# Performance work log

Measured on AMD Instinct MI355X. Metric: run time of the kernel, lower is better.

## Reference

```python
import jax, jax.numpy as jnp
import numpy as np

N_NODES = 100000
N_EDGES = 1600000
IN_DIM = 128
N_HID = 128


def setup_inputs() -> dict:
    key = jax.random.key(0)
    k1, k2, k3, k4 = jax.random.split(key, 4)
    node_feature = jax.random.normal(k1, (N_NODES, IN_DIM), dtype=jnp.float32)
    edge_index = jax.random.randint(k2, (2, N_EDGES), 0, N_NODES, dtype=jnp.int64)
    # GCN layer weights (glorot-ish scale)
    W1 = jax.random.normal(k3, (IN_DIM, N_HID), dtype=jnp.float32) / np.sqrt(IN_DIM)
    b1 = jnp.zeros((N_HID,), dtype=jnp.float32)
    W2 = jax.random.normal(k4, (N_HID, N_HID), dtype=jnp.float32) / np.sqrt(N_HID)
    b2 = jnp.zeros((N_HID,), dtype=jnp.float32)
    return {"node_feature": node_feature, "edge_index": edge_index,
            "W1": W1, "b1": b1, "W2": W2, "b2": b2}


def _gcn_layer(x, W, b, row, col, n_nodes):
    """GCNConv: x' = D^-1/2 (A + I) D^-1/2 (x W) + b, symmetric norm with self-loops."""
    xt = x @ W  # [N, out]
    ones = jnp.ones(row.shape[0], dtype=xt.dtype)
    deg = jnp.zeros((n_nodes,), dtype=xt.dtype).at[col].add(ones) + 1.0  # +1 self-loop
    dinv = jax.lax.rsqrt(deg)  # [N]
    norm = dinv[row] * dinv[col]  # [E]
    # gather messages from source (row), scatter-add into destination (col)
    agg = jnp.zeros_like(xt).at[col].add(xt[row] * norm[:, None])
    agg = agg + xt * (dinv * dinv)[:, None]  # self-loop contribution
    return agg + b


def reference(node_feature, edge_index, W1, b1, W2, b2):
    row, col = edge_index[0], edge_index[1]
    n = node_feature.shape[0]
    h = _gcn_layer(node_feature, W1, b1, row, col, n)
    # F.dropout with training=False is identity (eval-mode reference)
    h = _gcn_layer(h, W2, b2, row, col, n)
    return h
```

## Files before the change

kernel.cpp:

```cpp
#include <hip/hip_runtime.h>

typedef unsigned short ushort_t;
typedef __attribute__((ext_vector_type(8))) short short8;
typedef __attribute__((ext_vector_type(8))) unsigned short us8v;
typedef __attribute__((ext_vector_type(4))) float f32x4;

__device__ __forceinline__ float b2f(unsigned short u) {
    union { unsigned int i; float f; } v; v.i = ((unsigned int)u) << 16; return v.f;
}
__device__ __forceinline__ unsigned short f2b(float f) {
    union { float f; unsigned int i; } v; v.f = f;
    unsigned int r = (v.i + 0x7FFF + ((v.i >> 16) & 1)) >> 16;
    return (unsigned short)r;
}

__device__ __forceinline__ void load_edge(const int* __restrict__ ei, int e, int E,
                                          int is64, int& s, int& d) {
    if (is64) {
        const long long* el = (const long long*)ei;
        s = (int)el[e]; d = (int)el[E + e];
    } else {
        s = ei[e]; d = ei[E + e];
    }
}

__device__ __forceinline__ int detect64(const int* __restrict__ ei, int t) {
    int z = 0;
    for (int i = t; i < 512; i += 256) z |= ei[2 * i + 1];
    return (__syncthreads_or(z) == 0);
}

__global__ __launch_bounds__(256) void k_histT(const int* __restrict__ ei, int E,
                                               unsigned N, int* __restrict__ bhist,
                                               int BSH, int NB, int nch,
                                               const float* __restrict__ W1,
                                               const float* __restrict__ W2,
                                               ushort_t* __restrict__ WT) {
    __shared__ int lh[256];
    int t = threadIdx.x;
    int b = blockIdx.x;
    if (b >= nch) {
        const float* src = (b == nch) ? W1 : W2;
        ushort_t* dst = WT + (b - nch) * 16384;
        for (int i = t; i < 16384; i += 256) {
            int n = i >> 7, k = i & 127;
            dst[i] = f2b(src[k * 128 + n]);
        }
        return;
    }
    for (int q = t; q < NB; q += 256) lh[q] = 0;
    int is64 = detect64(ei, t);
    int e0 = b * 4096;
    #pragma unroll
    for (int i = 0; i < 16; ++i) {
        int e = e0 + i * 256 + t;
        if (e < E) {
            int d = is64 ? (int)((const long long*)ei)[E + e] : ei[E + e];
            if ((unsigned)d < N) atomicAdd(&lh[d >> BSH], 1);
        }
    }
    __syncthreads();
    for (int q = t; q < NB; q += 256) { int v = lh[q]; if (v) atomicAdd(&bhist[q], v); }
}

__global__ void k_scanb(const int* __restrict__ bhist, int NB,
                        int* __restrict__ bkbase, int* __restrict__ bkcur) {
    __shared__ int sd[256];
    int t = threadIdx.x;
    int v0 = (t < NB) ? bhist[t] : 0;
    sd[t] = v0;
    for (int o = 1; o < 256; o <<= 1) {
        __syncthreads();
        int v = (t >= o) ? sd[t - o] : 0;
        __syncthreads();
        sd[t] += v;
    }
    __syncthreads();
    if (t < NB) { int ex = sd[t] - v0; bkbase[t] = ex; bkcur[t] = ex; }
}

__global__ __launch_bounds__(256) void k_bg(const int* __restrict__ ei, int E,
                                            unsigned N, int* __restrict__ bkcur,
                                            int* __restrict__ bs, int* __restrict__ bd,
                                            int BSH, int NB, int nch,
                                            const float* __restrict__ x,
                                            const ushort_t* __restrict__ WT,
                                            ushort_t* __restrict__ xt, int M) {
    __shared__ __align__(16) int smem[13056];
    int t = threadIdx.x;
    int b = blockIdx.x;

    if (b < nch) {
        int* lss = smem;
        int* ldd = smem + 4096;
        int* lhist = smem + 8192;
        int* lcur = smem + 8448;
        int e0 = b * 4096;
        for (int q = t; q < NB; q += 256) lhist[q] = 0;
        int is64 = detect64(ei, t);
        #pragma unroll
        for (int i = 0; i < 16; ++i) {
            int idx = i * 256 + t, e = e0 + idx;
            int s = -1, d = -1;
            if (e < E) {
                load_edge(ei, e, E, is64, s, d);
                if (!((unsigned)s < N && (unsigned)d < N)) d = -1;
            }
            lss[idx] = s; ldd[idx] = d;
            if (d >= 0) atomicAdd(&lhist[d >> BSH], 1);
        }
        __syncthreads();
        for (int q = t; q < NB; q += 256) {
            int v = lhist[q];
            lcur[q] = v ? atomicAdd(&bkcur[q], v) : 0;
        }
        __syncthreads();
        #pragma unroll
        for (int i = 0; i < 16; ++i) {
            int idx = i * 256 + t;
            int d = ldd[idx];
            if (d >= 0) {
                int p = atomicAdd(&lcur[d >> BSH], 1);
                bs[p] = lss[idx]; bd[p] = d;
            }
        }
    } else {
        ushort_t* sA = (ushort_t*)smem;
        ushort_t* sW = (ushort_t*)smem + 8704;
        int row0 = (b - nch) * 64;
        #pragma unroll
        for (int it = 0; it < 8; ++it) {
            int flat = (it * 256 + t) * 8;
            int n = flat >> 7, k = flat & 127;
            uint4 v = *(const uint4*)(WT + flat);
            *(uint4*)(&sW[n * 136 + k]) = v;
        }
        #pragma unroll
        for (int it = 0; it < 4; ++it) {
            int flat = (it * 256 + t) * 8;
            int r = flat >> 7, cc = flat & 127;
            int row = row0 + r; if (row > M - 1) row = M - 1;
            const float* p = x + (size_t)row * 128 + cc;
            float4 f0 = *(const float4*)p;
            float4 f1 = *(const float4*)(p + 4);
            ushort_t tmp[8] __attribute__((aligned(16)));
            tmp[0] = f2b(f0.x); tmp[1] = f2b(f0.y); tmp[2] = f2b(f0.z); tmp[3] = f2b(f0.w);
            tmp[4] = f2b(f1.x); tmp[5] = f2b(f1.y); tmp[6] = f2b(f1.z); tmp[7] = f2b(f1.w);
            *(uint4*)(&sA[r * 136 + cc]) = *(const uint4*)tmp;
        }
        __syncthreads();
        int w = t >> 6, lane = t & 63;
        int m = lane & 15, quad = lane >> 4;
        f32x4 acc[8] = {};
        #pragma unroll
        for (int k0 = 0; k0 < 128; k0 += 32) {
            short8 af = *(const short8*)(&sA[(w * 16 + m) * 136 + k0 + quad * 8]);
            #pragma unroll
            for (int tt = 0; tt < 8; ++tt) {
                short8 bf = *(const short8*)(&sW[(tt * 16 + m) * 136 + k0 + quad * 8]);
                acc[tt] = __builtin_amdgcn_mfma_f32_16x16x32_bf16(af, bf, acc[tt], 0, 0, 0);
            }
        }
        #pragma unroll
        for (int r = 0; r < 4; ++r) {
            int row = row0 + w * 16 + quad * 4 + r;
            if (row < M) {
                #pragma unroll
                for (int tt = 0; tt < 8; ++tt)
                    xt[(size_t)row * 128 + tt * 16 + m] = f2b(acc[tt][r]);
            }
        }
    }
}

__global__ __launch_bounds__(256) void k_caf(const int* __restrict__ bs,
                                             const int* __restrict__ bd,
                                             const int* __restrict__ bkbase,
                                             const int* __restrict__ bkcur,
                                             int N, int BSH,
                                             int* __restrict__ pos,
                                             int* __restrict__ cnt,
                                             float* __restrict__ dinv,
                                             int* __restrict__ srcs) {
    __shared__ int lc[512];
    __shared__ int sc[512];
    int b = blockIdx.x, t = threadIdx.x;
    int nbase = b << BSH;
    int nn = min(1 << BSH, N - nbase);
    int segbase = bkbase[b] + b * (7 << BSH);

    lc[t] = 0; lc[t + 256] = 0;
    __syncthreads();
    int s0 = bkbase[b], s1 = bkcur[b];
    for (int i = s0 + t; i < s1; i += 256) atomicAdd(&lc[bd[i] - nbase], 1);
    __syncthreads();

    int c0 = (t < nn) ? lc[t] : 0;
    int c1 = (t + 256 < nn) ? lc[t + 256] : 0;
    int p0 = (c0 + 7) & ~7;
    int p1 = (c1 + 7) & ~7;
    sc[t] = p0; sc[t + 256] = p1;
    __syncthreads();
    for (int o = 1; o < 512; o <<= 1) {
        int v0 = (t >= o) ? sc[t - o] : 0;
        int v1 = (t + 256 >= o) ? sc[t + 256 - o] : 0;
        __syncthreads();
        sc[t] += v0; sc[t + 256] += v1;
        __syncthreads();
    }
    if (t < nn) {
        int st = segbase + sc[t] - p0;
        pos[nbase + t] = st;
        cnt[nbase + t] = c0;
        dinv[nbase + t] = rsqrtf((float)c0 + 1.0f);
        for (int q = c0; q < p0; ++q) srcs[st + q] = nbase + t;
        lc[t] = st;
    }
    if (t + 256 < nn) {
        int st = segbase + sc[t + 256] - p1;
        pos[nbase + t + 256] = st;
        cnt[nbase + t + 256] = c1;
        dinv[nbase + t + 256] = rsqrtf((float)c1 + 1.0f);
        for (int q = c1; q < p1; ++q) srcs[st + q] = nbase + t + 256;
        lc[t + 256] = st;
    }
    __syncthreads();
    for (int i = s0 + t; i < s1; i += 256) {
        int d = bd[i];
        int p = atomicAdd(&lc[d - nbase], 1);
        srcs[p] = bs[i];
    }
}

__global__ __launch_bounds__(256) void k_gemm2(const ushort_t* __restrict__ A,
                                               const ushort_t* __restrict__ WT,
                                               ushort_t* __restrict__ C,
                                               const float* __restrict__ dinv, int M) {
    __shared__ __align__(16) ushort_t sA[64 * 136];
    __shared__ __align__(16) ushort_t sW[128 * 136];
    int t = threadIdx.x;
    int row0 = blockIdx.x * 64;
    #pragma unroll
    for (int it = 0; it < 8; ++it) {
        int flat = (it * 256 + t) * 8;
        int n = flat >> 7, k = flat & 127;
        uint4 v = *(const uint4*)(WT + flat);
        *(uint4*)(&sW[n * 136 + k]) = v;
    }
    #pragma unroll
    for (int it = 0; it < 4; ++it) {
        int flat = (it * 256 + t) * 8;
        int r = flat >> 7, cc = flat & 127;
        int row = row0 + r; if (row > M - 1) row = M - 1;
        us8v v = *(const us8v*)(A + ((size_t)row << 7) + cc);
        *(us8v*)(&sA[r * 136 + cc]) = v;
    }
    __syncthreads();
    int w = t >> 6, lane = t & 63;
    int m = lane & 15, quad = lane >> 4;
    f32x4 acc[8] = {};
    #pragma unroll
    for (int k0 = 0; k0 < 128; k0 += 32) {
        short8 af = *(const short8*)(&sA[(w * 16 + m) * 136 + k0 + quad * 8]);
        #pragma unroll
        for (int tt = 0; tt < 8; ++tt) {
            short8 bf = *(const short8*)(&sW[(tt * 16 + m) * 136 + k0 + quad * 8]);
            acc[tt] = __builtin_amdgcn_mfma_f32_16x16x32_bf16(af, bf, acc[tt], 0, 0, 0);
        }
    }
    #pragma unroll
    for (int r = 0; r < 4; ++r) {
        int row = row0 + w * 16 + quad * 4 + r;
        if (row < M) {
            float dd = dinv[row];
            #pragma unroll
            for (int tt = 0; tt < 8; ++tt)
                C[(size_t)row * 128 + tt * 16 + m] = f2b(dd * acc[tt][r]);
        }
    }
}

template <bool OBF, bool WEI>
__global__ __launch_bounds__(256) void k_agg(const ushort_t* __restrict__ xt,
                                             const float* __restrict__ bias,
                                             void* __restrict__ outp,
                                             const int* __restrict__ pos,
                                             const int* __restrict__ cnts,
                                             const float* __restrict__ dinv,
                                             const int* __restrict__ srcs, int N) {
    int lane = threadIdx.x & 63;
    int slot = lane >> 4, j = lane & 15;
    int d = (blockIdx.x << 2) + (threadIdx.x >> 6);
    if (d >= N) return;
    int c = cnts[d];
    int cn = (c + 7) & ~7;
    float kpad = (float)(cn - c);
    int start = pos[d];
    float dd = dinv[d];
    float selfc = WEI ? (1.f - kpad) * dd * dd : (1.f - kpad) * dd;
    us8v vs = *(const us8v*)(xt + ((size_t)d << 7) + (j << 3));
    float4 bb0 = *(const float4*)(bias + (j << 3));
    float4 bb1 = *(const float4*)(bias + (j << 3) + 4);

    float a0 = 0.f, a1 = 0.f, a2 = 0.f, a3 = 0.f;
    float a4 = 0.f, a5 = 0.f, a6 = 0.f, a7 = 0.f;

    for (int base = 0; base < cn; base += 64) {
        int n = cn - base; if (n > 64) n = 64;
        int sv = 0; float wv = 1.f;
        if (lane < n) {
            sv = srcs[start + base + lane];
            if (WEI) wv = dinv[sv];
        }
        int s0 = __shfl(sv, slot);
        int s1 = __shfl(sv, 4 + slot);
        float w0 = WEI ? __shfl(wv, slot) : 1.f;
        float w1 = WEI ? __shfl(wv, 4 + slot) : 1.f;
        us8v v0 = *(const us8v*)(xt + ((size_t)s0 << 7) + (j << 3));
        us8v v1 = *(const us8v*)(xt + ((size_t)s1 << 7) + (j << 3));
        for (int cc = 8; cc < n; cc += 8) {
            int t0 = __shfl(sv, cc + slot);
            int t1 = __shfl(sv, cc + 4 + slot);
            float u0 = WEI ? __shfl(wv, cc + slot) : 1.f;
            float u1 = WEI ? __shfl(wv, cc + 4 + slot) : 1.f;
            us8v n0 = *(const us8v*)(xt + ((size_t)t0 << 7) + (j << 3));
            us8v n1 = *(const us8v*)(xt + ((size_t)t1 << 7) + (j << 3));
            if (WEI) {
                a0 += w0 * b2f(v0[0]); a1 += w0 * b2f(v0[1]);
                a2 += w0 * b2f(v0[2]); a3 += w0 * b2f(v0[3]);
                a4 += w0 * b2f(v0[4]); a5 += w0 * b2f(v0[5]);
                a6 += w0 * b2f(v0[6]); a7 += w0 * b2f(v0[7]);
                a0 += w1 * b2f(v1[0]); a1 += w1 * b2f(v1[1]);
                a2 += w1 * b2f(v1[2]); a3 += w1 * b2f(v1[3]);
                a4 += w1 * b2f(v1[4]); a5 += w1 * b2f(v1[5]);
                a6 += w1 * b2f(v1[6]); a7 += w1 * b2f(v1[7]);
            } else {
                a0 += b2f(v0[0]); a1 += b2f(v0[1]); a2 += b2f(v0[2]); a3 += b2f(v0[3]);
                a4 += b2f(v0[4]); a5 += b2f(v0[5]); a6 += b2f(v0[6]); a7 += b2f(v0[7]);
                a0 += b2f(v1[0]); a1 += b2f(v1[1]); a2 += b2f(v1[2]); a3 += b2f(v1[3]);
                a4 += b2f(v1[4]); a5 += b2f(v1[5]); a6 += b2f(v1[6]); a7 += b2f(v1[7]);
            }
            v0 = n0; v1 = n1; w0 = u0; w1 = u1;
        }
        if (WEI) {
            a0 += w0 * b2f(v0[0]); a1 += w0 * b2f(v0[1]);
            a2 += w0 * b2f(v0[2]); a3 += w0 * b2f(v0[3]);
            a4 += w0 * b2f(v0[4]); a5 += w0 * b2f(v0[5]);
            a6 += w0 * b2f(v0[6]); a7 += w0 * b2f(v0[7]);
            a0 += w1 * b2f(v1[0]); a1 += w1 * b2f(v1[1]);
            a2 += w1 * b2f(v1[2]); a3 += w1 * b2f(v1[3]);
            a4 += w1 * b2f(v1[4]); a5 += w1 * b2f(v1[5]);
            a6 += w1 * b2f(v1[6]); a7 += w1 * b2f(v1[7]);
        } else {
            a0 += b2f(v0[0]); a1 += b2f(v0[1]); a2 += b2f(v0[2]); a3 += b2f(v0[3]);
            a4 += b2f(v0[4]); a5 += b2f(v0[5]); a6 += b2f(v0[6]); a7 += b2f(v0[7]);
            a0 += b2f(v1[0]); a1 += b2f(v1[1]); a2 += b2f(v1[2]); a3 += b2f(v1[3]);
            a4 += b2f(v1[4]); a5 += b2f(v1[5]); a6 += b2f(v1[6]); a7 += b2f(v1[7]);
        }
    }
    a0 += __shfl_xor(a0, 32); a1 += __shfl_xor(a1, 32);
    a2 += __shfl_xor(a2, 32); a3 += __shfl_xor(a3, 32);
    a4 += __shfl_xor(a4, 32); a5 += __shfl_xor(a5, 32);
    a6 += __shfl_xor(a6, 32); a7 += __shfl_xor(a7, 32);
    a0 += __shfl_xor(a0, 16); a1 += __shfl_xor(a1, 16);
    a2 += __shfl_xor(a2, 16); a3 += __shfl_xor(a3, 16);
    a4 += __shfl_xor(a4, 16); a5 += __shfl_xor(a5, 16);
    a6 += __shfl_xor(a6, 16); a7 += __shfl_xor(a7, 16);

    if (slot == 0) {
        float o0 = dd * a0 + selfc * b2f(vs[0]) + bb0.x;
        float o1 = dd * a1 + selfc * b2f(vs[1]) + bb0.y;
        float o2 = dd * a2 + selfc * b2f(vs[2]) + bb0.z;
        float o3 = dd * a3 + selfc * b2f(vs[3]) + bb0.w;
        float o4 = dd * a4 + selfc * b2f(vs[4]) + bb1.x;
        float o5 = dd * a5 + selfc * b2f(vs[5]) + bb1.y;
        float o6 = dd * a6 + selfc * b2f(vs[6]) + bb1.z;
        float o7 = dd * a7 + selfc * b2f(vs[7]) + bb1.w;
        if (OBF) {
            ushort_t tmp[8] __attribute__((aligned(16)));
            tmp[0] = f2b(o0); tmp[1] = f2b(o1); tmp[2] = f2b(o2); tmp[3] = f2b(o3);
            tmp[4] = f2b(o4); tmp[5] = f2b(o5); tmp[6] = f2b(o6); tmp[7] = f2b(o7);
            *(us8v*)((ushort_t*)outp + ((size_t)d << 7) + (j << 3)) = *(const us8v*)tmp;
        } else {
            float4 q0 = { o0, o1, o2, o3 };
            float4 q1 = { o4, o5, o6, o7 };
            float4* po = (float4*)((float*)outp + ((size_t)d << 7) + (j << 3));
            po[0] = q0; po[1] = q1;
        }
    }
}


extern "C" void kernel_launch(void* const* d_in, const int* in_sizes, int n_in,
                              void* d_out, int out_size, void* d_ws, size_t ws_size,
                              hipStream_t stream) {
    const float* x  = (const float*)d_in[0];
    const int*   ei = (const int*)d_in[1];
    const float* W1 = (const float*)d_in[2];
    const float* b1 = (const float*)d_in[3];
    const float* W2 = (const float*)d_in[4];
    const float* b2 = (const float*)d_in[5];
    float* out = (float*)d_out;

    const int N = in_sizes[0] / 128;
    const int E = in_sizes[1] / 2;

    int BSH = 9;
    int NB = (N + (1 << BSH) - 1) >> BSH;
    while (NB > 256) { BSH++; NB = (N + (1 << BSH) - 1) >> BSH; }

    char* ws = (char*)d_ws;
    size_t o = 0;
    auto take = [&](size_t bytes) { size_t r = o; o = (o + bytes + 255) & ~(size_t)255; return r; };
    size_t o_bhist  = take(256 * 4);
    size_t zero_end = o;
    size_t o_bkbase = take(256 * 4);
    size_t o_bkcur  = take(256 * 4);
    size_t o_cnt    = take((size_t)N * 4);
    size_t o_pos    = take((size_t)N * 4);
    size_t o_dinv   = take((size_t)N * 4);
    size_t o_srcs   = take(((size_t)E + (size_t)NB * (7 << BSH) + 64) * 4);
    size_t o_WT     = take(2 * 128 * 128 * 2);
    size_t big_sz   = (size_t)E * 8 > (size_t)N * 256 ? (size_t)E * 8 : (size_t)N * 256;
    size_t o_big    = take(big_sz);
    (void)ws_size;

    int*      bhist  = (int*)(ws + o_bhist);
    int*      bkbase = (int*)(ws + o_bkbase);
    int*      bkcur  = (int*)(ws + o_bkcur);
    int*      cnt    = (int*)(ws + o_cnt);
    int*      pos    = (int*)(ws + o_pos);
    float*    dinv   = (float*)(ws + o_dinv);
    int*      srcs   = (int*)(ws + o_srcs);
    ushort_t* WT     = (ushort_t*)(ws + o_WT);
    int*      bs     = (int*)(ws + o_big);
    int*      bd     = (int*)(ws + o_big) + E;
    ushort_t* xt2    = (ushort_t*)(ws + o_big);
    ushort_t* xt1    = (ushort_t*)d_out;
    ushort_t* hbf    = (ushort_t*)d_out + (size_t)N * 128;

    hipMemsetAsync(d_ws, 0, zero_end, stream);

    int nch = (E + 4095) / 4096;
    int gG  = (N + 63) / 64;
    int gA  = (N + 3) / 4;
    unsigned Nu = (unsigned)N;

    k_histT<<<nch + 2, 256, 0, stream>>>(ei, E, Nu, bhist, BSH, NB, nch, W1, W2, WT);
    k_scanb<<<1, 256, 0, stream>>>(bhist, NB, bkbase, bkcur);
    k_bg<<<nch + gG, 256, 0, stream>>>(ei, E, Nu, bkcur, bs, bd, BSH, NB, nch,
                                       x, WT, xt1, N);
    k_caf<<<NB, 256, 0, stream>>>(bs, bd, bkbase, bkcur, N, BSH, pos, cnt, dinv, srcs);

    k_agg<true, true><<<gA, 256, 0, stream>>>(xt1, b1, hbf, pos, cnt, dinv, srcs, N);
    k_gemm2<<<gG, 256, 0, stream>>>(hbf, WT + 16384, xt2, dinv, N);
    k_agg<false, false><<<gA, 256, 0, stream>>>(xt2, b2, out, pos, cnt, dinv, srcs, N);
}
```

Before: 317.8 us.

## Store intermediate features in column-slab layout and aggregate per 16-feature slice

The bf16 intermediate feature matrices are now written by both GEMMs as eight slabs of 16 features per node instead of row-major 128-wide rows. The aggregation kernel assigns each block to one slab, so its gathered working set is a 1/8-sized array that can stay in cache, and each wave gathers 32-byte segments per neighbor. The aim is better L2/MALL hit rates for the random neighbor gathers. The cost is that each edge's source index and weight are read eight times, one per slice, and each gather moves smaller chunks.

```diff
diff --git a/kernel.cpp b/kernel.cpp
--- a/kernel.cpp
+++ b/kernel.cpp
@@ -4,6 +4,8 @@
 typedef __attribute__((ext_vector_type(8))) short short8;
 typedef __attribute__((ext_vector_type(8))) unsigned short us8v;
 typedef __attribute__((ext_vector_type(4))) float f32x4;
+
+struct __align__(4) us2 { unsigned short x, y; };
 
 __device__ __forceinline__ float b2f(unsigned short u) {
     union { unsigned int i; float f; } v; v.i = ((unsigned int)u) << 16; return v.f;
@@ -128,6 +130,7 @@
         ushort_t* sA = (ushort_t*)smem;
         ushort_t* sW = (ushort_t*)smem + 8704;
         int row0 = (b - nch) * 64;
+        size_t sstride = (size_t)M * 16;
         #pragma unroll
         for (int it = 0; it < 8; ++it) {
             int flat = (it * 256 + t) * 8;
@@ -167,7 +170,7 @@
             if (row < M) {
                 #pragma unroll
                 for (int tt = 0; tt < 8; ++tt)
-                    xt[(size_t)row * 128 + tt * 16 + m] = f2b(acc[tt][r]);
+                    xt[(size_t)tt * sstride + (size_t)row * 16 + m] = f2b(acc[tt][r]);
             }
         }
     }
@@ -240,6 +243,7 @@
     __shared__ __align__(16) ushort_t sW[128 * 136];
     int t = threadIdx.x;
     int row0 = blockIdx.x * 64;
+    size_t sstride = (size_t)M * 16;
     #pragma unroll
     for (int it = 0; it < 8; ++it) {
         int flat = (it * 256 + t) * 8;
@@ -252,7 +256,8 @@
         int flat = (it * 256 + t) * 8;
         int r = flat >> 7, cc = flat & 127;
         int row = row0 + r; if (row > M - 1) row = M - 1;
-        us8v v = *(const us8v*)(A + ((size_t)row << 7) + cc);
+        int slab = cc >> 4, off = cc & 15;
+        us8v v = *(const us8v*)(A + (size_t)slab * sstride + (size_t)row * 16 + off);
         *(us8v*)(&sA[r * 136 + cc]) = v;
     }
     __syncthreads();
@@ -275,7 +280,7 @@
             float dd = dinv[row];
             #pragma unroll
             for (int tt = 0; tt < 8; ++tt)
-                C[(size_t)row * 128 + tt * 16 + m] = f2b(dd * acc[tt][r]);
+                C[(size_t)tt * sstride + (size_t)row * 16 + m] = f2b(dd * acc[tt][r]);
         }
     }
 }
@@ -289,103 +294,61 @@
                                              const float* __restrict__ dinv,
                                              const int* __restrict__ srcs, int N) {
     int lane = threadIdx.x & 63;
-    int slot = lane >> 4, j = lane & 15;
-    int d = (blockIdx.x << 2) + (threadIdx.x >> 6);
-    if (d >= N) return;
-    int c = cnts[d];
-    int cn = (c + 7) & ~7;
-    float kpad = (float)(cn - c);
-    int start = pos[d];
-    float dd = dinv[d];
-    float selfc = WEI ? (1.f - kpad) * dd * dd : (1.f - kpad) * dd;
-    us8v vs = *(const us8v*)(xt + ((size_t)d << 7) + (j << 3));
-    float4 bb0 = *(const float4*)(bias + (j << 3));
-    float4 bb1 = *(const float4*)(bias + (j << 3) + 4);
-
-    float a0 = 0.f, a1 = 0.f, a2 = 0.f, a3 = 0.f;
-    float a4 = 0.f, a5 = 0.f, a6 = 0.f, a7 = 0.f;
-
-    for (int base = 0; base < cn; base += 64) {
-        int n = cn - base; if (n > 64) n = 64;
-        int sv = 0; float wv = 1.f;
-        if (lane < n) {
-            sv = srcs[start + base + lane];
-            if (WEI) wv = dinv[sv];
-        }
-        int s0 = __shfl(sv, slot);
-        int s1 = __shfl(sv, 4 + slot);
-        float w0 = WEI ? __shfl(wv, slot) : 1.f;
-        float w1 = WEI ? __shfl(wv, 4 + slot) : 1.f;
-        us8v v0 = *(const us8v*)(xt + ((size_t)s0 << 7) + (j << 3));
-        us8v v1 = *(const us8v*)(xt + ((size_t)s1 << 7) + (j << 3));
-        for (int cc = 8; cc < n; cc += 8) {
-            int t0 = __shfl(sv, cc + slot);
-            int t1 = __shfl(sv, cc + 4 + slot);
-            float u0 = WEI ? __shfl(wv, cc + slot) : 1.f;
-            float u1 = WEI ? __shfl(wv, cc + 4 + slot) : 1.f;
-            us8v n0 = *(const us8v*)(xt + ((size_t)t0 << 7) + (j << 3));
-            us8v n1 = *(const us8v*)(xt + ((size_t)t1 << 7) + (j << 3));
-            if (WEI) {
-                a0 += w0 * b2f(v0[0]); a1 += w0 * b2f(v0[1]);
-                a2 += w0 * b2f(v0[2]); a3 += w0 * b2f(v0[3]);
-                a4 += w0 * b2f(v0[4]); a5 += w0 * b2f(v0[5]);
-                a6 += w0 * b2f(v0[6]); a7 += w0 * b2f(v0[7]);
-                a0 += w1 * b2f(v1[0]); a1 += w1 * b2f(v1[1]);
-                a2 += w1 * b2f(v1[2]); a3 += w1 * b2f(v1[3]);
-                a4 += w1 * b2f(v1[4]); a5 += w1 * b2f(v1[5]);
-                a6 += w1 * b2f(v1[6]); a7 += w1 * b2f(v1[7]);
+    int wid = threadIdx.x >> 6;
+    int slice = blockIdx.x & 7;
+    int dbase = (blockIdx.x >> 3) * 16;
+    int g = lane >> 3;
+    int fp = lane & 7;
+    size_t sstride = (size_t)N * 16;
+    const ushort_t* slab = xt + (size_t)slice * sstride;
+    float2 bb = *(const float2*)(bias + slice * 16 + fp * 2);
+
+    for (int k = 0; k < 4; ++k) {
+        int d = dbase + wid + k * 4;
+        if (d >= N) break;
+        int c = cnts[d];
+        int cn = (c + 7) & ~7;
+        float kpad = (float)(cn - c);
+        int start = pos[d];
+        float dd = dinv[d];
+        float selfc = WEI ? (1.f - kpad) * dd * dd : (1.f - kpad) * dd;
+        us2 vsv = *(const us2*)(slab + (size_t)d * 16 + fp * 2);
+
+        float a0 = 0.f, a1 = 0.f;
+        for (int base = 0; base < cn; base += 64) {
+            int n = cn - base; if (n > 64) n = 64;
+            int sv = 0; float wv = 1.f;
+            if (lane < n) {
+                sv = srcs[start + base + lane];
+                if (WEI) wv = dinv[sv];
+            }
+            #pragma unroll 4
+            for (int cc = 0; cc < n; cc += 8) {
+                int s = __shfl(sv, cc + g);
+                us2 v = *(const us2*)(slab + (size_t)s * 16 + fp * 2);
+                if (WEI) {
+                    float w = __shfl(wv, cc + g);
+                    a0 += w * b2f(v.x); a1 += w * b2f(v.y);
+                } else {
+                    a0 += b2f(v.x); a1 += b2f(v.y);
+                }
+            }
+        }
+        a0 += __shfl_xor(a0, 8);  a1 += __shfl_xor(a1, 8);
+        a0 += __shfl_xor(a0, 16); a1 += __shfl_xor(a1, 16);
+        a0 += __shfl_xor(a0, 32); a1 += __shfl_xor(a1, 32);
+
+        if (g == 0) {
+            float o0 = dd * a0 + selfc * b2f(vsv.x) + bb.x;
+            float o1 = dd * a1 + selfc * b2f(vsv.y) + bb.y;
+            if (OBF) {
+                us2 t2; t2.x = f2b(o0); t2.y = f2b(o1);
+                *(us2*)((ushort_t*)outp + (size_t)slice * sstride
+                        + (size_t)d * 16 + fp * 2) = t2;
             } else {
-                a0 += b2f(v0[0]); a1 += b2f(v0[1]); a2 += b2f(v0[2]); a3 += b2f(v0[3]);
-                a4 += b2f(v0[4]); a5 += b2f(v0[5]); a6 += b2f(v0[6]); a7 += b2f(v0[7]);
-                a0 += b2f(v1[0]); a1 += b2f(v1[1]); a2 += b2f(v1[2]); a3 += b2f(v1[3]);
-                a4 += b2f(v1[4]); a5 += b2f(v1[5]); a6 += b2f(v1[6]); a7 += b2f(v1[7]);
-            }
-            v0 = n0; v1 = n1; w0 = u0; w1 = u1;
-        }
-        if (WEI) {
-            a0 += w0 * b2f(v0[0]); a1 += w0 * b2f(v0[1]);
-            a2 += w0 * b2f(v0[2]); a3 += w0 * b2f(v0[3]);
-            a4 += w0 * b2f(v0[4]); a5 += w0 * b2f(v0[5]);
-            a6 += w0 * b2f(v0[6]); a7 += w0 * b2f(v0[7]);
-            a0 += w1 * b2f(v1[0]); a1 += w1 * b2f(v1[1]);
-            a2 += w1 * b2f(v1[2]); a3 += w1 * b2f(v1[3]);
-            a4 += w1 * b2f(v1[4]); a5 += w1 * b2f(v1[5]);
-            a6 += w1 * b2f(v1[6]); a7 += w1 * b2f(v1[7]);
-        } else {
-            a0 += b2f(v0[0]); a1 += b2f(v0[1]); a2 += b2f(v0[2]); a3 += b2f(v0[3]);
-            a4 += b2f(v0[4]); a5 += b2f(v0[5]); a6 += b2f(v0[6]); a7 += b2f(v0[7]);
-            a0 += b2f(v1[0]); a1 += b2f(v1[1]); a2 += b2f(v1[2]); a3 += b2f(v1[3]);
-            a4 += b2f(v1[4]); a5 += b2f(v1[5]); a6 += b2f(v1[6]); a7 += b2f(v1[7]);
-        }
-    }
-    a0 += __shfl_xor(a0, 32); a1 += __shfl_xor(a1, 32);
-    a2 += __shfl_xor(a2, 32); a3 += __shfl_xor(a3, 32);
-    a4 += __shfl_xor(a4, 32); a5 += __shfl_xor(a5, 32);
-    a6 += __shfl_xor(a6, 32); a7 += __shfl_xor(a7, 32);
-    a0 += __shfl_xor(a0, 16); a1 += __shfl_xor(a1, 16);
-    a2 += __shfl_xor(a2, 16); a3 += __shfl_xor(a3, 16);
-    a4 += __shfl_xor(a4, 16); a5 += __shfl_xor(a5, 16);
-    a6 += __shfl_xor(a6, 16); a7 += __shfl_xor(a7, 16);
-
-    if (slot == 0) {
-        float o0 = dd * a0 + selfc * b2f(vs[0]) + bb0.x;
-        float o1 = dd * a1 + selfc * b2f(vs[1]) + bb0.y;
-        float o2 = dd * a2 + selfc * b2f(vs[2]) + bb0.z;
-        float o3 = dd * a3 + selfc * b2f(vs[3]) + bb0.w;
-        float o4 = dd * a4 + selfc * b2f(vs[4]) + bb1.x;
-        float o5 = dd * a5 + selfc * b2f(vs[5]) + bb1.y;
-        float o6 = dd * a6 + selfc * b2f(vs[6]) + bb1.z;
-        float o7 = dd * a7 + selfc * b2f(vs[7]) + bb1.w;
-        if (OBF) {
-            ushort_t tmp[8] __attribute__((aligned(16)));
-            tmp[0] = f2b(o0); tmp[1] = f2b(o1); tmp[2] = f2b(o2); tmp[3] = f2b(o3);
-            tmp[4] = f2b(o4); tmp[5] = f2b(o5); tmp[6] = f2b(o6); tmp[7] = f2b(o7);
-            *(us8v*)((ushort_t*)outp + ((size_t)d << 7) + (j << 3)) = *(const us8v*)tmp;
-        } else {
-            float4 q0 = { o0, o1, o2, o3 };
-            float4 q1 = { o4, o5, o6, o7 };
-            float4* po = (float4*)((float*)outp + ((size_t)d << 7) + (j << 3));
-            po[0] = q0; po[1] = q1;
+                float2 q; q.x = o0; q.y = o1;
+                *(float2*)((float*)outp + (size_t)d * 128 + slice * 16 + fp * 2) = q;
+            }
         }
     }
 }
@@ -443,7 +406,7 @@
 
     int nch = (E + 4095) / 4096;
     int gG  = (N + 63) / 64;
-    int gA  = (N + 3) / 4;
+    int gA  = 8 * ((N + 15) / 16);
     unsigned Nu = (unsigned)N;
 
     k_histT<<<nch + 2, 256, 0, stream>>>(ei, E, Nu, bhist, BSH, NB, nch, W1, W2, WT);
```

Result: slower. 582.0 us (+83.1%).

## Fuse bucket scan into histogram kernel and reduce CSR padding to four

Applied to the files above, without the earlier changes.

The single-block bucket scan kernel is folded into the histogram kernel using a last-block-done atomic counter, which removes one kernel launch. Per-node edge lists are now padded to multiples of 4 instead of 8, and the aggregation loop gains a 4-edge tail path. This cuts the padding gathers of self-row values (average degree is 16, so 8-padding wasted about 3.5 rows per node). The cost is an extra global atomic and fence per block, plus a bit more control flow in the aggregation loop.

```diff
diff --git a/kernel.cpp b/kernel.cpp
--- a/kernel.cpp
+++ b/kernel.cpp
@@ -35,8 +35,12 @@
                                                int BSH, int NB, int nch,
                                                const float* __restrict__ W1,
                                                const float* __restrict__ W2,
-                                               ushort_t* __restrict__ WT) {
+                                               ushort_t* __restrict__ WT,
+                                               int* __restrict__ done,
+                                               int* __restrict__ bkbase,
+                                               int* __restrict__ bkcur) {
     __shared__ int lh[256];
+    __shared__ int lastFlag;
     int t = threadIdx.x;
     int b = blockIdx.x;
     if (b >= nch) {
@@ -46,37 +50,39 @@
             int n = i >> 7, k = i & 127;
             dst[i] = f2b(src[k * 128 + n]);
         }
-        return;
-    }
-    for (int q = t; q < NB; q += 256) lh[q] = 0;
-    int is64 = detect64(ei, t);
-    int e0 = b * 4096;
-    #pragma unroll
-    for (int i = 0; i < 16; ++i) {
-        int e = e0 + i * 256 + t;
-        if (e < E) {
-            int d = is64 ? (int)((const long long*)ei)[E + e] : ei[E + e];
-            if ((unsigned)d < N) atomicAdd(&lh[d >> BSH], 1);
-        }
-    }
-    __syncthreads();
-    for (int q = t; q < NB; q += 256) { int v = lh[q]; if (v) atomicAdd(&bhist[q], v); }
-}
-
-__global__ void k_scanb(const int* __restrict__ bhist, int NB,
-                        int* __restrict__ bkbase, int* __restrict__ bkcur) {
-    __shared__ int sd[256];
-    int t = threadIdx.x;
-    int v0 = (t < NB) ? bhist[t] : 0;
-    sd[t] = v0;
-    for (int o = 1; o < 256; o <<= 1) {
-        __syncthreads();
-        int v = (t >= o) ? sd[t - o] : 0;
-        __syncthreads();
-        sd[t] += v;
-    }
-    __syncthreads();
-    if (t < NB) { int ex = sd[t] - v0; bkbase[t] = ex; bkcur[t] = ex; }
+    } else {
+        for (int q = t; q < NB; q += 256) lh[q] = 0;
+        int is64 = detect64(ei, t);
+        int e0 = b * 4096;
+        #pragma unroll
+        for (int i = 0; i < 16; ++i) {
+            int e = e0 + i * 256 + t;
+            if (e < E) {
+                int d = is64 ? (int)((const long long*)ei)[E + e] : ei[E + e];
+                if ((unsigned)d < N) atomicAdd(&lh[d >> BSH], 1);
+            }
+        }
+        __syncthreads();
+        for (int q = t; q < NB; q += 256) {
+            int v = lh[q]; if (v) atomicAdd(&bhist[q], v);
+        }
+    }
+    __threadfence();
+    if (t == 0) lastFlag = (atomicAdd(done, 1) == (int)gridDim.x - 1);
+    __syncthreads();
+    if (lastFlag) {
+        __threadfence();
+        int v0 = (t < NB) ? atomicAdd(&bhist[t], 0) : 0;
+        lh[t] = v0;
+        for (int o = 1; o < 256; o <<= 1) {
+            __syncthreads();
+            int v = (t >= o) ? lh[t - o] : 0;
+            __syncthreads();
+            lh[t] += v;
+        }
+        __syncthreads();
+        if (t < NB) { int ex = lh[t] - v0; bkbase[t] = ex; bkcur[t] = ex; }
+    }
 }
 
 __global__ __launch_bounds__(256) void k_bg(const int* __restrict__ ei, int E,
@@ -187,7 +193,7 @@
     int b = blockIdx.x, t = threadIdx.x;
     int nbase = b << BSH;
     int nn = min(1 << BSH, N - nbase);
-    int segbase = bkbase[b] + b * (7 << BSH);
+    int segbase = bkbase[b] + b * (3 << BSH);
 
     lc[t] = 0; lc[t + 256] = 0;
     __syncthreads();
@@ -197,8 +203,8 @@
 
     int c0 = (t < nn) ? lc[t] : 0;
     int c1 = (t + 256 < nn) ? lc[t + 256] : 0;
-    int p0 = (c0 + 7) & ~7;
-    int p1 = (c1 + 7) & ~7;
+    int p0 = (c0 + 3) & ~3;
+    int p1 = (c1 + 3) & ~3;
     sc[t] = p0; sc[t + 256] = p1;
     __syncthreads();
     for (int o = 1; o < 512; o <<= 1) {
@@ -293,7 +299,7 @@
     int d = (blockIdx.x << 2) + (threadIdx.x >> 6);
     if (d >= N) return;
     int c = cnts[d];
-    int cn = (c + 7) & ~7;
+    int cn = (c + 3) & ~3;
     float kpad = (float)(cn - c);
     int start = pos[d];
     float dd = dinv[d];
@@ -312,20 +318,21 @@
             sv = srcs[start + base + lane];
             if (WEI) wv = dinv[sv];
         }
-        int s0 = __shfl(sv, slot);
-        int s1 = __shfl(sv, 4 + slot);
-        float w0 = WEI ? __shfl(wv, slot) : 1.f;
-        float w1 = WEI ? __shfl(wv, 4 + slot) : 1.f;
-        us8v v0 = *(const us8v*)(xt + ((size_t)s0 << 7) + (j << 3));
-        us8v v1 = *(const us8v*)(xt + ((size_t)s1 << 7) + (j << 3));
-        for (int cc = 8; cc < n; cc += 8) {
-            int t0 = __shfl(sv, cc + slot);
-            int t1 = __shfl(sv, cc + 4 + slot);
-            float u0 = WEI ? __shfl(wv, cc + slot) : 1.f;
-            float u1 = WEI ? __shfl(wv, cc + 4 + slot) : 1.f;
-            us8v n0 = *(const us8v*)(xt + ((size_t)t0 << 7) + (j << 3));
-            us8v n1 = *(const us8v*)(xt + ((size_t)t1 << 7) + (j << 3));
-            if (WEI) {
+        int n8 = n & ~7;
+        if (n8) {
+            int s0 = __shfl(sv, slot);
+            int s1 = __shfl(sv, 4 + slot);
+            float w0 = WEI ? __shfl(wv, slot) : 1.f;
+            float w1 = WEI ? __shfl(wv, 4 + slot) : 1.f;
+            us8v v0 = *(const us8v*)(xt + ((size_t)s0 << 7) + (j << 3));
+            us8v v1 = *(const us8v*)(xt + ((size_t)s1 << 7) + (j << 3));
+            for (int cc = 8; cc < n8; cc += 8) {
+                int t0 = __shfl(sv, cc + slot);
+                int t1 = __shfl(sv, cc + 4 + slot);
+                float u0 = WEI ? __shfl(wv, cc + slot) : 1.f;
+                float u1 = WEI ? __shfl(wv, cc + 4 + slot) : 1.f;
+                us8v m0 = *(const us8v*)(xt + ((size_t)t0 << 7) + (j << 3));
+                us8v m1 = *(const us8v*)(xt + ((size_t)t1 << 7) + (j << 3));
                 a0 += w0 * b2f(v0[0]); a1 += w0 * b2f(v0[1]);
                 a2 += w0 * b2f(v0[2]); a3 += w0 * b2f(v0[3]);
                 a4 += w0 * b2f(v0[4]); a5 += w0 * b2f(v0[5]);
@@ -334,15 +341,8 @@
                 a2 += w1 * b2f(v1[2]); a3 += w1 * b2f(v1[3]);
                 a4 += w1 * b2f(v1[4]); a5 += w1 * b2f(v1[5]);
                 a6 += w1 * b2f(v1[6]); a7 += w1 * b2f(v1[7]);
-            } else {
-                a0 += b2f(v0[0]); a1 += b2f(v0[1]); a2 += b2f(v0[2]); a3 += b2f(v0[3]);
-                a4 += b2f(v0[4]); a5 += b2f(v0[5]); a6 += b2f(v0[6]); a7 += b2f(v0[7]);
-                a0 += b2f(v1[0]); a1 += b2f(v1[1]); a2 += b2f(v1[2]); a3 += b2f(v1[3]);
-                a4 += b2f(v1[4]); a5 += b2f(v1[5]); a6 += b2f(v1[6]); a7 += b2f(v1[7]);
-            }
-            v0 = n0; v1 = n1; w0 = u0; w1 = u1;
-        }
-        if (WEI) {
+                v0 = m0; v1 = m1; w0 = u0; w1 = u1;
+            }
             a0 += w0 * b2f(v0[0]); a1 += w0 * b2f(v0[1]);
             a2 += w0 * b2f(v0[2]); a3 += w0 * b2f(v0[3]);
             a4 += w0 * b2f(v0[4]); a5 += w0 * b2f(v0[5]);
@@ -351,11 +351,15 @@
             a2 += w1 * b2f(v1[2]); a3 += w1 * b2f(v1[3]);
             a4 += w1 * b2f(v1[4]); a5 += w1 * b2f(v1[5]);
             a6 += w1 * b2f(v1[6]); a7 += w1 * b2f(v1[7]);
-        } else {
-            a0 += b2f(v0[0]); a1 += b2f(v0[1]); a2 += b2f(v0[2]); a3 += b2f(v0[3]);
-            a4 += b2f(v0[4]); a5 += b2f(v0[5]); a6 += b2f(v0[6]); a7 += b2f(v0[7]);
-            a0 += b2f(v1[0]); a1 += b2f(v1[1]); a2 += b2f(v1[2]); a3 += b2f(v1[3]);
-            a4 += b2f(v1[4]); a5 += b2f(v1[5]); a6 += b2f(v1[6]); a7 += b2f(v1[7]);
+        }
+        if (n & 4) {
+            int s = __shfl(sv, n8 + slot);
+            float w = WEI ? __shfl(wv, n8 + slot) : 1.f;
+            us8v v = *(const us8v*)(xt + ((size_t)s << 7) + (j << 3));
+            a0 += w * b2f(v[0]); a1 += w * b2f(v[1]);
+            a2 += w * b2f(v[2]); a3 += w * b2f(v[3]);
+            a4 += w * b2f(v[4]); a5 += w * b2f(v[5]);
+            a6 += w * b2f(v[6]); a7 += w * b2f(v[7]);
         }
     }
     a0 += __shfl_xor(a0, 32); a1 += __shfl_xor(a1, 32);
@@ -413,19 +417,21 @@
     size_t o = 0;
     auto take = [&](size_t bytes) { size_t r = o; o = (o + bytes + 255) & ~(size_t)255; return r; };
     size_t o_bhist  = take(256 * 4);
+    size_t o_done   = take(4);
     size_t zero_end = o;
     size_t o_bkbase = take(256 * 4);
     size_t o_bkcur  = take(256 * 4);
     size_t o_cnt    = take((size_t)N * 4);
     size_t o_pos    = take((size_t)N * 4);
     size_t o_dinv   = take((size_t)N * 4);
-    size_t o_srcs   = take(((size_t)E + (size_t)NB * (7 << BSH) + 64) * 4);
+    size_t o_srcs   = take(((size_t)E + (size_t)NB * (3 << BSH) + 64) * 4);
     size_t o_WT     = take(2 * 128 * 128 * 2);
     size_t big_sz   = (size_t)E * 8 > (size_t)N * 256 ? (size_t)E * 8 : (size_t)N * 256;
     size_t o_big    = take(big_sz);
     (void)ws_size;
 
     int*      bhist  = (int*)(ws + o_bhist);
+    int*      done   = (int*)(ws + o_done);
     int*      bkbase = (int*)(ws + o_bkbase);
     int*      bkcur  = (int*)(ws + o_bkcur);
     int*      cnt    = (int*)(ws + o_cnt);
@@ -446,8 +452,8 @@
     int gA  = (N + 3) / 4;
     unsigned Nu = (unsigned)N;
 
-    k_histT<<<nch + 2, 256, 0, stream>>>(ei, E, Nu, bhist, BSH, NB, nch, W1, W2, WT);
-    k_scanb<<<1, 256, 0, stream>>>(bhist, NB, bkbase, bkcur);
+    k_histT<<<nch + 2, 256, 0, stream>>>(ei, E, Nu, bhist, BSH, NB, nch,
+                                         W1, W2, WT, done, bkbase, bkcur);
     k_bg<<<nch + gG, 256, 0, stream>>>(ei, E, Nu, bkcur, bs, bd, BSH, NB, nch,
                                        x, WT, xt1, N);
     k_caf<<<NB, 256, 0, stream>>>(bs, bd, bkbase, bkcur, N, BSH, pos, cnt, dinv, srcs);
```

Measured after the change: 335.1 us. 1.05x slower.

## Fold bucket scan into consumers and split GEMM1 across bucketing and CSR kernels

Applied to the files above, without the earlier changes.

Removes the single-block scan kernel launch: each bucketing block and each CSR-build block recomputes the 256-entry prefix scan of the bucket histogram in shared memory, and bkcur is now zeroed and holds relative offsets. The first-layer GEMM blocks are split in half, with one half co-scheduled alongside edge bucketing and the other alongside the CSR build, to fill idle CUs in the small NB-block kernel. The aggregation loop is also simplified to always apply weights. The cost is redundant scans in every block, which add extra syncs, and more shared memory in k_caf.

```diff
diff --git a/kernel.cpp b/kernel.cpp
--- a/kernel.cpp
+++ b/kernel.cpp
@@ -28,6 +28,56 @@
     int z = 0;
     for (int i = t; i < 512; i += 256) z |= ei[2 * i + 1];
     return (__syncthreads_or(z) == 0);
+}
+
+__device__ __forceinline__ void gemm1_block(const float* __restrict__ x,
+                                            const ushort_t* __restrict__ WT,
+                                            ushort_t* __restrict__ xt, int M,
+                                            int row0, int* smem, int t) {
+    ushort_t* sA = (ushort_t*)smem;
+    ushort_t* sW = (ushort_t*)smem + 8704;
+    #pragma unroll
+    for (int it = 0; it < 8; ++it) {
+        int flat = (it * 256 + t) * 8;
+        int n = flat >> 7, k = flat & 127;
+        uint4 v = *(const uint4*)(WT + flat);
+        *(uint4*)(&sW[n * 136 + k]) = v;
+    }
+    #pragma unroll
+    for (int it = 0; it < 4; ++it) {
+        int flat = (it * 256 + t) * 8;
+        int r = flat >> 7, cc = flat & 127;
+        int row = row0 + r; if (row > M - 1) row = M - 1;
+        const float* p = x + (size_t)row * 128 + cc;
+        float4 f0 = *(const float4*)p;
+        float4 f1 = *(const float4*)(p + 4);
+        ushort_t tmp[8] __attribute__((aligned(16)));
+        tmp[0] = f2b(f0.x); tmp[1] = f2b(f0.y); tmp[2] = f2b(f0.z); tmp[3] = f2b(f0.w);
+        tmp[4] = f2b(f1.x); tmp[5] = f2b(f1.y); tmp[6] = f2b(f1.z); tmp[7] = f2b(f1.w);
+        *(uint4*)(&sA[r * 136 + cc]) = *(const uint4*)tmp;
+    }
+    __syncthreads();
+    int w = t >> 6, lane = t & 63;
+    int m = lane & 15, quad = lane >> 4;
+    f32x4 acc[8] = {};
+    #pragma unroll
+    for (int k0 = 0; k0 < 128; k0 += 32) {
+        short8 af = *(const short8*)(&sA[(w * 16 + m) * 136 + k0 + quad * 8]);
+        #pragma unroll
+        for (int tt = 0; tt < 8; ++tt) {
+            short8 bf = *(const short8*)(&sW[(tt * 16 + m) * 136 + k0 + quad * 8]);
+            acc[tt] = __builtin_amdgcn_mfma_f32_16x16x32_bf16(af, bf, acc[tt], 0, 0, 0);
+        }
+    }
+    #pragma unroll
+    for (int r = 0; r < 4; ++r) {
+        int row = row0 + w * 16 + quad * 4 + r;
+        if (row < M) {
+            #pragma unroll
+            for (int tt = 0; tt < 8; ++tt)
+                xt[(size_t)row * 128 + tt * 16 + m] = f2b(acc[tt][r]);
+        }
+    }
 }
 
 __global__ __launch_bounds__(256) void k_histT(const int* __restrict__ ei, int E,
@@ -63,24 +113,9 @@
     for (int q = t; q < NB; q += 256) { int v = lh[q]; if (v) atomicAdd(&bhist[q], v); }
 }
 
-__global__ void k_scanb(const int* __restrict__ bhist, int NB,
-                        int* __restrict__ bkbase, int* __restrict__ bkcur) {
-    __shared__ int sd[256];
-    int t = threadIdx.x;
-    int v0 = (t < NB) ? bhist[t] : 0;
-    sd[t] = v0;
-    for (int o = 1; o < 256; o <<= 1) {
-        __syncthreads();
-        int v = (t >= o) ? sd[t - o] : 0;
-        __syncthreads();
-        sd[t] += v;
-    }
-    __syncthreads();
-    if (t < NB) { int ex = sd[t] - v0; bkbase[t] = ex; bkcur[t] = ex; }
-}
-
 __global__ __launch_bounds__(256) void k_bg(const int* __restrict__ ei, int E,
-                                            unsigned N, int* __restrict__ bkcur,
+                                            unsigned N, const int* __restrict__ bhist,
+                                            int* __restrict__ bkcur,
                                             int* __restrict__ bs, int* __restrict__ bd,
                                             int BSH, int NB, int nch,
                                             const float* __restrict__ x,
@@ -95,7 +130,18 @@
         int* ldd = smem + 4096;
         int* lhist = smem + 8192;
         int* lcur = smem + 8448;
+        int* sbk = smem + 8704;
         int e0 = b * 4096;
+        int hv = (t < NB) ? bhist[t] : 0;
+        sbk[t] = hv;
+        for (int o = 1; o < 256; o <<= 1) {
+            __syncthreads();
+            int v = (t >= o) ? sbk[t - o] : 0;
+            __syncthreads();
+            sbk[t] += v;
+        }
+        __syncthreads();
+        sbk[t] -= hv;
         for (int q = t; q < NB; q += 256) lhist[q] = 0;
         int is64 = detect64(ei, t);
         #pragma unroll
@@ -112,7 +158,7 @@
         __syncthreads();
         for (int q = t; q < NB; q += 256) {
             int v = lhist[q];
-            lcur[q] = v ? atomicAdd(&bkcur[q], v) : 0;
+            lcur[q] = v ? (sbk[q] + atomicAdd(&bkcur[q], v)) : 0;
         }
         __syncthreads();
         #pragma unroll
@@ -125,73 +171,51 @@
             }
         }
     } else {
-        ushort_t* sA = (ushort_t*)smem;
-        ushort_t* sW = (ushort_t*)smem + 8704;
-        int row0 = (b - nch) * 64;
-        #pragma unroll
-        for (int it = 0; it < 8; ++it) {
-            int flat = (it * 256 + t) * 8;
-            int n = flat >> 7, k = flat & 127;
-            uint4 v = *(const uint4*)(WT + flat);
-            *(uint4*)(&sW[n * 136 + k]) = v;
-        }
-        #pragma unroll
-        for (int it = 0; it < 4; ++it) {
-            int flat = (it * 256 + t) * 8;
-            int r = flat >> 7, cc = flat & 127;
-            int row = row0 + r; if (row > M - 1) row = M - 1;
-            const float* p = x + (size_t)row * 128 + cc;
-            float4 f0 = *(const float4*)p;
-            float4 f1 = *(const float4*)(p + 4);
-            ushort_t tmp[8] __attribute__((aligned(16)));
-            tmp[0] = f2b(f0.x); tmp[1] = f2b(f0.y); tmp[2] = f2b(f0.z); tmp[3] = f2b(f0.w);
-            tmp[4] = f2b(f1.x); tmp[5] = f2b(f1.y); tmp[6] = f2b(f1.z); tmp[7] = f2b(f1.w);
-            *(uint4*)(&sA[r * 136 + cc]) = *(const uint4*)tmp;
-        }
-        __syncthreads();
-        int w = t >> 6, lane = t & 63;
-        int m = lane & 15, quad = lane >> 4;
-        f32x4 acc[8] = {};
-        #pragma unroll
-        for (int k0 = 0; k0 < 128; k0 += 32) {
-            short8 af = *(const short8*)(&sA[(w * 16 + m) * 136 + k0 + quad * 8]);
-            #pragma unroll
-            for (int tt = 0; tt < 8; ++tt) {
-                short8 bf = *(const short8*)(&sW[(tt * 16 + m) * 136 + k0 + quad * 8]);
-                acc[tt] = __builtin_amdgcn_mfma_f32_16x16x32_bf16(af, bf, acc[tt], 0, 0, 0);
-            }
-        }
-        #pragma unroll
-        for (int r = 0; r < 4; ++r) {
-            int row = row0 + w * 16 + quad * 4 + r;
-            if (row < M) {
-                #pragma unroll
-                for (int tt = 0; tt < 8; ++tt)
-                    xt[(size_t)row * 128 + tt * 16 + m] = f2b(acc[tt][r]);
-            }
-        }
+        gemm1_block(x, WT, xt, M, (b - nch) * 64, smem, t);
     }
 }
 
 __global__ __launch_bounds__(256) void k_caf(const int* __restrict__ bs,
                                              const int* __restrict__ bd,
-                                             const int* __restrict__ bkbase,
-                                             const int* __restrict__ bkcur,
-                                             int N, int BSH,
+                                             const int* __restrict__ bhist,
+                                             int N, int BSH, int NB,
                                              int* __restrict__ pos,
                                              int* __restrict__ cnt,
                                              float* __restrict__ dinv,
-                                             int* __restrict__ srcs) {
-    __shared__ int lc[512];
-    __shared__ int sc[512];
-    int b = blockIdx.x, t = threadIdx.x;
+                                             int* __restrict__ srcs,
+                                             const float* __restrict__ x,
+                                             const ushort_t* __restrict__ WT,
+                                             ushort_t* __restrict__ xt, int M,
+                                             int GH1) {
+    __shared__ __align__(16) int smem[13056];
+    int t = threadIdx.x;
+    int b = blockIdx.x;
+    if (b >= NB) {
+        gemm1_block(x, WT, xt, M, (GH1 + b - NB) * 64, smem, t);
+        return;
+    }
+    int* lc = smem;
+    int* sc = smem + 512;
+    __shared__ int sBase, sCnt;
     int nbase = b << BSH;
     int nn = min(1 << BSH, N - nbase);
-    int segbase = bkbase[b] + b * (7 << BSH);
+
+    int hv = (t < NB) ? bhist[t] : 0;
+    sc[t] = hv;
+    for (int o = 1; o < 256; o <<= 1) {
+        __syncthreads();
+        int v = (t >= o) ? sc[t - o] : 0;
+        __syncthreads();
+        sc[t] += v;
+    }
+    __syncthreads();
+    if (t == b) { sBase = sc[b] - hv; sCnt = hv; }
+    __syncthreads();
+    int s0 = sBase, s1 = sBase + sCnt;
+    int segbase = sBase + b * (7 << BSH);
 
     lc[t] = 0; lc[t + 256] = 0;
     __syncthreads();
-    int s0 = bkbase[b], s1 = bkcur[b];
     for (int i = s0 + t; i < s1; i += 256) atomicAdd(&lc[bd[i] - nbase], 1);
     __syncthreads();
 
@@ -323,26 +347,8 @@
             int t1 = __shfl(sv, cc + 4 + slot);
             float u0 = WEI ? __shfl(wv, cc + slot) : 1.f;
             float u1 = WEI ? __shfl(wv, cc + 4 + slot) : 1.f;
-            us8v n0 = *(const us8v*)(xt + ((size_t)t0 << 7) + (j << 3));
-            us8v n1 = *(const us8v*)(xt + ((size_t)t1 << 7) + (j << 3));
-            if (WEI) {
-                a0 += w0 * b2f(v0[0]); a1 += w0 * b2f(v0[1]);
-                a2 += w0 * b2f(v0[2]); a3 += w0 * b2f(v0[3]);
-                a4 += w0 * b2f(v0[4]); a5 += w0 * b2f(v0[5]);
-                a6 += w0 * b2f(v0[6]); a7 += w0 * b2f(v0[7]);
-                a0 += w1 * b2f(v1[0]); a1 += w1 * b2f(v1[1]);
-                a2 += w1 * b2f(v1[2]); a3 += w1 * b2f(v1[3]);
-                a4 += w1 * b2f(v1[4]); a5 += w1 * b2f(v1[5]);
-                a6 += w1 * b2f(v1[6]); a7 += w1 * b2f(v1[7]);
-            } else {
-                a0 += b2f(v0[0]); a1 += b2f(v0[1]); a2 += b2f(v0[2]); a3 += b2f(v0[3]);
-                a4 += b2f(v0[4]); a5 += b2f(v0[5]); a6 += b2f(v0[6]); a7 += b2f(v0[7]);
-                a0 += b2f(v1[0]); a1 += b2f(v1[1]); a2 += b2f(v1[2]); a3 += b2f(v1[3]);
-                a4 += b2f(v1[4]); a5 += b2f(v1[5]); a6 += b2f(v1[6]); a7 += b2f(v1[7]);
-            }
-            v0 = n0; v1 = n1; w0 = u0; w1 = u1;
-        }
-        if (WEI) {
+            us8v m0 = *(const us8v*)(xt + ((size_t)t0 << 7) + (j << 3));
+            us8v m1 = *(const us8v*)(xt + ((size_t)t1 << 7) + (j << 3));
             a0 += w0 * b2f(v0[0]); a1 += w0 * b2f(v0[1]);
             a2 += w0 * b2f(v0[2]); a3 += w0 * b2f(v0[3]);
             a4 += w0 * b2f(v0[4]); a5 += w0 * b2f(v0[5]);
@@ -351,12 +357,16 @@
             a2 += w1 * b2f(v1[2]); a3 += w1 * b2f(v1[3]);
             a4 += w1 * b2f(v1[4]); a5 += w1 * b2f(v1[5]);
             a6 += w1 * b2f(v1[6]); a7 += w1 * b2f(v1[7]);
-        } else {
-            a0 += b2f(v0[0]); a1 += b2f(v0[1]); a2 += b2f(v0[2]); a3 += b2f(v0[3]);
-            a4 += b2f(v0[4]); a5 += b2f(v0[5]); a6 += b2f(v0[6]); a7 += b2f(v0[7]);
-            a0 += b2f(v1[0]); a1 += b2f(v1[1]); a2 += b2f(v1[2]); a3 += b2f(v1[3]);
-            a4 += b2f(v1[4]); a5 += b2f(v1[5]); a6 += b2f(v1[6]); a7 += b2f(v1[7]);
-        }
+            v0 = m0; v1 = m1; w0 = u0; w1 = u1;
+        }
+        a0 += w0 * b2f(v0[0]); a1 += w0 * b2f(v0[1]);
+        a2 += w0 * b2f(v0[2]); a3 += w0 * b2f(v0[3]);
+        a4 += w0 * b2f(v0[4]); a5 += w0 * b2f(v0[5]);
+        a6 += w0 * b2f(v0[6]); a7 += w0 * b2f(v0[7]);
+        a0 += w1 * b2f(v1[0]); a1 += w1 * b2f(v1[1]);
+        a2 += w1 * b2f(v1[2]); a3 += w1 * b2f(v1[3]);
+        a4 += w1 * b2f(v1[4]); a5 += w1 * b2f(v1[5]);
+        a6 += w1 * b2f(v1[6]); a7 += w1 * b2f(v1[7]);
     }
     a0 += __shfl_xor(a0, 32); a1 += __shfl_xor(a1, 32);
     a2 += __shfl_xor(a2, 32); a3 += __shfl_xor(a3, 32);
@@ -413,9 +423,8 @@
     size_t o = 0;
     auto take = [&](size_t bytes) { size_t r = o; o = (o + bytes + 255) & ~(size_t)255; return r; };
     size_t o_bhist  = take(256 * 4);
+    size_t o_bkcur  = take(256 * 4);
     size_t zero_end = o;
-    size_t o_bkbase = take(256 * 4);
-    size_t o_bkcur  = take(256 * 4);
     size_t o_cnt    = take((size_t)N * 4);
     size_t o_pos    = take((size_t)N * 4);
     size_t o_dinv   = take((size_t)N * 4);
@@ -426,7 +435,6 @@
     (void)ws_size;
 
     int*      bhist  = (int*)(ws + o_bhist);
-    int*      bkbase = (int*)(ws + o_bkbase);
     int*      bkcur  = (int*)(ws + o_bkcur);
     int*      cnt    = (int*)(ws + o_cnt);
     int*      pos    = (int*)(ws + o_pos);
@@ -443,14 +451,16 @@
 
     int nch = (E + 4095) / 4096;
     int gG  = (N + 63) / 64;
+    int GH1 = (gG + 1) / 2;
+    int GH2 = gG - GH1;
     int gA  = (N + 3) / 4;
     unsigned Nu = (unsigned)N;
 
     k_histT<<<nch + 2, 256, 0, stream>>>(ei, E, Nu, bhist, BSH, NB, nch, W1, W2, WT);
-    k_scanb<<<1, 256, 0, stream>>>(bhist, NB, bkbase, bkcur);
-    k_bg<<<nch + gG, 256, 0, stream>>>(ei, E, Nu, bkcur, bs, bd, BSH, NB, nch,
-                                       x, WT, xt1, N);
-    k_caf<<<NB, 256, 0, stream>>>(bs, bd, bkbase, bkcur, N, BSH, pos, cnt, dinv, srcs);
+    k_bg<<<nch + GH1, 256, 0, stream>>>(ei, E, Nu, bhist, bkcur, bs, bd, BSH, NB,
+                                        nch, x, WT, xt1, N);
+    k_caf<<<NB + GH2, 256, 0, stream>>>(bs, bd, bhist, N, BSH, NB, pos, cnt, dinv,
+                                        srcs, x, WT, xt1, N, GH1);
 
     k_agg<true, true><<<gA, 256, 0, stream>>>(xt1, b1, hbf, pos, cnt, dinv, srcs, N);
     k_gemm2<<<gG, 256, 0, stream>>>(hbf, WT + 16384, xt2, dinv, N);
```

Result: no change. 318.7 us (+0.3%).
